# Optimization experiments

Measured on AMD Instinct MI355X. Metric: run time of the kernel, lower is better.

## Reference

```python
import jax, jax.numpy as jnp
import numpy as np

N, IN_DIM, OUT_DIM, E = 50000, 64, 64, 800000


def setup_inputs() -> dict:
    key = jax.random.key(0)
    k1, k2, k3, k4 = jax.random.split(key, 4)
    x = jax.random.normal(k1, (N, IN_DIM), dtype=jnp.float32)
    edge_index = jax.random.randint(k2, (2, E), 0, N, dtype=jnp.int64)
    # nn.Linear(in_dim, out_dim): weight [out, in], bias [out]
    bound = 1.0 / np.sqrt(IN_DIM)
    W = jax.random.uniform(k3, (OUT_DIM, IN_DIM), minval=-bound, maxval=bound, dtype=jnp.float32)
    b = jax.random.uniform(k4, (OUT_DIM,), minval=-bound, maxval=bound, dtype=jnp.float32)
    return {"x": x, "edge_index": edge_index, "W": W, "b": b}


def reference(x, edge_index, W, b):
    row, col = edge_index[0], edge_index[1]
    n = x.shape[0]
    # deg = bincount(row, minlength=N) + 1e-6, shape [N, 1]
    deg = jnp.zeros((n,), dtype=jnp.float32).at[row].add(1.0)[:, None] + 1e-6
    # agg[row] += x[col]  (gather + scatter-add)
    agg = jnp.zeros_like(x).at[row].add(x[col])
    agg = agg / deg
    return agg @ W.T + b
```

## Files before the change

kernel.cpp:

```cpp
#include <hip/hip_runtime.h>
#include <hip/hip_bf16.h>

#define N_NODES 50000
#define DIM 64
#define N_EDGES 800000
#define CAP 64
#define NTHR 256


static __device__ inline unsigned int f2bf(float f) {
    __hip_bfloat16 h = __float2bfloat16(f);
    return (unsigned int)*reinterpret_cast<unsigned short*>(&h);
}
static __device__ inline float bf_lo(unsigned int u) { return __uint_as_float(u << 16); }
static __device__ inline float bf_hi(unsigned int u) { return __uint_as_float(u & 0xffff0000u); }

__global__ __launch_bounds__(NTHR) void place_conv_kernel(
    const int* __restrict__ ei, const float* __restrict__ x,
    int* __restrict__ count, unsigned short* __restrict__ xb, int* csr)
{
    int tid = blockIdx.x * NTHR + threadIdx.x;
    int row = ei[tid], col = ei[N_EDGES + tid];
    int pos = atomicAdd(&count[row], 1);
    float4 v = ((const float4*)x)[tid];
    ushort4 u;
    u.x = (unsigned short)f2bf(v.x); u.y = (unsigned short)f2bf(v.y);
    u.z = (unsigned short)f2bf(v.z); u.w = (unsigned short)f2bf(v.w);
    ((ushort4*)xb)[tid] = u;
    if (pos < CAP) csr[row * CAP + pos] = col;
}

__global__ __launch_bounds__(NTHR) void agg_kernel(
    const unsigned short* __restrict__ xb, const int* __restrict__ count,
    const int* csr, const float* __restrict__ W, const float* __restrict__ bias,
    float* out)
{
    __shared__ uint4  Wb[512];
    __shared__ float  bs[DIM];
    __shared__ float4 rows4[4][16];

    int t = threadIdx.x;
    for (int m = t; m < 512; m += NTHR) {
        int o = m & 63, j8 = m >> 6;
        const float* wr = W + o * DIM + j8 * 8;
        uint4 uw;
        uw.x = f2bf(wr[0]) | (f2bf(wr[1]) << 16);
        uw.y = f2bf(wr[2]) | (f2bf(wr[3]) << 16);
        uw.z = f2bf(wr[4]) | (f2bf(wr[5]) << 16);
        uw.w = f2bf(wr[6]) | (f2bf(wr[7]) << 16);
        Wb[m] = uw;
    }
    if (t < DIM) bs[t] = bias[t];
    __syncthreads();

    int w   = t >> 6;
    int l   = t & 63;
    int sub = l & 7;
    int grp = l >> 3;
    int r   = blockIdx.x * 4 + w;

    int deg = count[r];
    int dc  = deg < CAP ? deg : CAP;
    int myc = csr[(size_t)r * CAP + l];

    const uint4* xbq = (const uint4*)xb;
    float s[8];
#pragma unroll
    for (int q = 0; q < 8; q++) s[q] = 0.f;

    for (int jb = 0; jb < dc; jb += 8) {
        int  j     = jb + grp;
        int  c     = __shfl(myc, j);
        bool valid = j < dc;
        int  cs    = valid ? c : 0;
        uint4 v = xbq[(size_t)cs * 8 + sub];
        if (valid) {
            s[0] += bf_lo(v.x); s[1] += bf_hi(v.x);
            s[2] += bf_lo(v.y); s[3] += bf_hi(v.y);
            s[4] += bf_lo(v.z); s[5] += bf_hi(v.z);
            s[6] += bf_lo(v.w); s[7] += bf_hi(v.w);
        }
    }
#pragma unroll
    for (int q = 0; q < 8; q++) {
        s[q] += __shfl_xor(s[q], 8);
        s[q] += __shfl_xor(s[q], 16);
        s[q] += __shfl_xor(s[q], 32);
    }

    float inv_d = 1.0f / ((float)deg + 1e-6f);
    if (grp == 0) {
        rows4[w][sub * 2]     = make_float4(s[0] * inv_d, s[1] * inv_d,
                                            s[2] * inv_d, s[3] * inv_d);
        rows4[w][sub * 2 + 1] = make_float4(s[4] * inv_d, s[5] * inv_d,
                                            s[6] * inv_d, s[7] * inv_d);
    }

    float acc = bs[l];
#pragma unroll
    for (int j8 = 0; j8 < 8; j8++) {
        uint4  wb = Wb[j8 * 64 + l];
        float4 r0 = rows4[w][2 * j8];
        float4 r1 = rows4[w][2 * j8 + 1];
        acc += r0.x * bf_lo(wb.x) + r0.y * bf_hi(wb.x)
             + r0.z * bf_lo(wb.y) + r0.w * bf_hi(wb.y)
             + r1.x * bf_lo(wb.z) + r1.y * bf_hi(wb.z)
             + r1.z * bf_lo(wb.w) + r1.w * bf_hi(wb.w);
    }
    out[(size_t)r * DIM + l] = acc;
}

extern "C" void kernel_launch(void* const* d_in, const int* in_sizes, int n_in,
                              void* d_out, int out_size, void* d_ws, size_t ws_size,
                              hipStream_t stream) {
    const float* x    = (const float*)d_in[0];
    const int*   ei   = (const int*)d_in[1];
    const float* W    = (const float*)d_in[2];
    const float* bias = (const float*)d_in[3];
    float* out = (float*)d_out;

    int*            count = (int*)d_ws;
    unsigned short* xb    = (unsigned short*)((char*)d_ws + 262144);
    int*            csr   = (int*)d_out;

    hipMemsetAsync(count, 0, N_NODES * sizeof(int), stream);
    place_conv_kernel<<<N_EDGES / NTHR, NTHR, 0, stream>>>(ei, x, count, xb, csr);
    agg_kernel<<<N_NODES / 4, NTHR, 0, stream>>>(xb, count, csr, W, bias, out);
}
```

Measured before the change: 153.4 us.

## Apply linear transform before aggregation and fuse GEMM into placement kernel

Uses linearity to compute x@W^T per node first, storing bf16 results, so aggregation only sums transformed rows, scales by inverse degree and adds the bias. The GEMM runs in extra blocks of the CSR-placement kernel, overlapping with the atomic edge placement. This drops the per-block W load and conversion plus the per-row matvec from the aggregation kernel. The trade-off is that bf16 rounding now applies to transformed features instead of raw x.

Measured after the change: 166.4 us. +8.5%, slower.

```diff
diff --git a/kernel.cpp b/kernel.cpp
--- a/kernel.cpp
+++ b/kernel.cpp
@@ -6,6 +6,9 @@
 #define N_EDGES 800000
 #define CAP 64
 #define NTHR 256
+#define GB_ROWS 64
+#define NGB 782
+#define PLACE_BLOCKS (N_EDGES / NTHR)
 
 
 static __device__ inline unsigned int f2bf(float f) {
@@ -15,44 +18,65 @@
 static __device__ inline float bf_lo(unsigned int u) { return __uint_as_float(u << 16); }
 static __device__ inline float bf_hi(unsigned int u) { return __uint_as_float(u & 0xffff0000u); }
 
-__global__ __launch_bounds__(NTHR) void place_conv_kernel(
+__global__ __launch_bounds__(NTHR) void place_gemm_kernel(
     const int* __restrict__ ei, const float* __restrict__ x,
-    int* __restrict__ count, unsigned short* __restrict__ xb, int* csr)
+    const float* __restrict__ W, int* __restrict__ count,
+    int* csr, unsigned short* __restrict__ xb)
 {
-    int tid = blockIdx.x * NTHR + threadIdx.x;
-    int row = ei[tid], col = ei[N_EDGES + tid];
-    int pos = atomicAdd(&count[row], 1);
-    float4 v = ((const float4*)x)[tid];
-    ushort4 u;
-    u.x = (unsigned short)f2bf(v.x); u.y = (unsigned short)f2bf(v.y);
-    u.z = (unsigned short)f2bf(v.z); u.w = (unsigned short)f2bf(v.w);
-    ((ushort4*)xb)[tid] = u;
-    if (pos < CAP) csr[row * CAP + pos] = col;
+    __shared__ float4 xs4[GB_ROWS * 16];
+    int t = threadIdx.x;
+
+    if (blockIdx.x < NGB) {
+        int R0 = blockIdx.x * GB_ROWS;
+        const float4* x4 = (const float4*)x;
+        for (int i = t; i < GB_ROWS * 16; i += NTHR) {
+            int g = R0 * 16 + i;
+            xs4[i] = (g < N_NODES * 16) ? x4[g] : make_float4(0.f, 0.f, 0.f, 0.f);
+        }
+        int w = t >> 6, l = t & 63;
+        uint4 wb[8];
+        const float4* Wf4 = (const float4*)W;
+#pragma unroll
+        for (int j8 = 0; j8 < 8; j8++) {
+            float4 a = Wf4[l * 16 + 2 * j8];
+            float4 c = Wf4[l * 16 + 2 * j8 + 1];
+            wb[j8].x = f2bf(a.x) | (f2bf(a.y) << 16);
+            wb[j8].y = f2bf(a.z) | (f2bf(a.w) << 16);
+            wb[j8].z = f2bf(c.x) | (f2bf(c.y) << 16);
+            wb[j8].w = f2bf(c.z) | (f2bf(c.w) << 16);
+        }
+        __syncthreads();
+#pragma unroll 4
+        for (int i = 0; i < 16; i++) {
+            int rl = i * 4 + w;
+            int r  = R0 + rl;
+            if (r >= N_NODES) break;
+            float acc = 0.f;
+#pragma unroll
+            for (int j8 = 0; j8 < 8; j8++) {
+                float4 x0 = xs4[rl * 16 + 2 * j8];
+                float4 x1 = xs4[rl * 16 + 2 * j8 + 1];
+                uint4  wq = wb[j8];
+                acc += x0.x * bf_lo(wq.x) + x0.y * bf_hi(wq.x)
+                     + x0.z * bf_lo(wq.y) + x0.w * bf_hi(wq.y)
+                     + x1.x * bf_lo(wq.z) + x1.y * bf_hi(wq.z)
+                     + x1.z * bf_lo(wq.w) + x1.w * bf_hi(wq.w);
+            }
+            xb[(size_t)r * DIM + l] = (unsigned short)f2bf(acc);
+        }
+    } else {
+        int e = (blockIdx.x - NGB) * NTHR + t;
+        int row = ei[e], col = ei[N_EDGES + e];
+        int pos = atomicAdd(&count[row], 1);
+        if (pos < CAP) csr[row * CAP + pos] = col;
+    }
 }
 
 __global__ __launch_bounds__(NTHR) void agg_kernel(
     const unsigned short* __restrict__ xb, const int* __restrict__ count,
-    const int* csr, const float* __restrict__ W, const float* __restrict__ bias,
-    float* out)
+    const int* csr, const float* __restrict__ bias, float* out)
 {
-    __shared__ uint4  Wb[512];
-    __shared__ float  bs[DIM];
-    __shared__ float4 rows4[4][16];
-
-    int t = threadIdx.x;
-    for (int m = t; m < 512; m += NTHR) {
-        int o = m & 63, j8 = m >> 6;
-        const float* wr = W + o * DIM + j8 * 8;
-        uint4 uw;
-        uw.x = f2bf(wr[0]) | (f2bf(wr[1]) << 16);
-        uw.y = f2bf(wr[2]) | (f2bf(wr[3]) << 16);
-        uw.z = f2bf(wr[4]) | (f2bf(wr[5]) << 16);
-        uw.w = f2bf(wr[6]) | (f2bf(wr[7]) << 16);
-        Wb[m] = uw;
-    }
-    if (t < DIM) bs[t] = bias[t];
-    __syncthreads();
-
+    int t   = threadIdx.x;
     int w   = t >> 6;
     int l   = t & 63;
     int sub = l & 7;
@@ -88,26 +112,17 @@
         s[q] += __shfl_xor(s[q], 32);
     }
 
-    float inv_d = 1.0f / ((float)deg + 1e-6f);
     if (grp == 0) {
-        rows4[w][sub * 2]     = make_float4(s[0] * inv_d, s[1] * inv_d,
-                                            s[2] * inv_d, s[3] * inv_d);
-        rows4[w][sub * 2 + 1] = make_float4(s[4] * inv_d, s[5] * inv_d,
-                                            s[6] * inv_d, s[7] * inv_d);
+        float inv_d = 1.0f / ((float)deg + 1e-6f);
+        float4 b0 = ((const float4*)bias)[2 * sub];
+        float4 b1 = ((const float4*)bias)[2 * sub + 1];
+        float4 o0 = make_float4(s[0] * inv_d + b0.x, s[1] * inv_d + b0.y,
+                                s[2] * inv_d + b0.z, s[3] * inv_d + b0.w);
+        float4 o1 = make_float4(s[4] * inv_d + b1.x, s[5] * inv_d + b1.y,
+                                s[6] * inv_d + b1.z, s[7] * inv_d + b1.w);
+        ((float4*)(out + (size_t)r * DIM))[2 * sub]     = o0;
+        ((float4*)(out + (size_t)r * DIM))[2 * sub + 1] = o1;
     }
-
-    float acc = bs[l];
-#pragma unroll
-    for (int j8 = 0; j8 < 8; j8++) {
-        uint4  wb = Wb[j8 * 64 + l];
-        float4 r0 = rows4[w][2 * j8];
-        float4 r1 = rows4[w][2 * j8 + 1];
-        acc += r0.x * bf_lo(wb.x) + r0.y * bf_hi(wb.x)
-             + r0.z * bf_lo(wb.y) + r0.w * bf_hi(wb.y)
-             + r1.x * bf_lo(wb.z) + r1.y * bf_hi(wb.z)
-             + r1.z * bf_lo(wb.w) + r1.w * bf_hi(wb.w);
-    }
-    out[(size_t)r * DIM + l] = acc;
 }
 
 extern "C" void kernel_launch(void* const* d_in, const int* in_sizes, int n_in,
@@ -124,6 +139,6 @@
     int*            csr   = (int*)d_out;
 
     hipMemsetAsync(count, 0, N_NODES * sizeof(int), stream);
-    place_conv_kernel<<<N_EDGES / NTHR, NTHR, 0, stream>>>(ei, x, count, xb, csr);
-    agg_kernel<<<N_NODES / 4, NTHR, 0, stream>>>(xb, count, csr, W, bias, out);
+    place_gemm_kernel<<<NGB + PLACE_BLOCKS, NTHR, 0, stream>>>(ei, x, W, count, csr, xb);
+    agg_kernel<<<N_NODES / 4, NTHR, 0, stream>>>(xb, count, csr, bias, out);
 }
```
